# Kernel tuning notes

Hardware: AMD Instinct MI355X
Metric: run time of the kernel (lower is better)

Reference implementation:

```python
import jax, jax.numpy as jnp
import numpy as np

N, E = 50000, 640000
FEAT, EMB, HID, B = 128, 128, 512, 32


def setup_inputs() -> dict:
    key = jax.random.key(0)
    ks = jax.random.split(key, 12)
    def w(k, shape, fan_in):
        return jax.random.normal(k, shape, dtype=jnp.float32) / np.sqrt(fan_in)
    return {
        "x": jax.random.normal(ks[0], (N, FEAT), dtype=jnp.float32),
        "edge_index": jax.random.randint(ks[1], (2, E), 0, N, dtype=jnp.int64),
        "last_hidden": jax.random.normal(ks[2], (1, B, HID), dtype=jnp.float32),
        "W1_rel": w(ks[3], (FEAT, EMB), FEAT),
        "W1_root": w(ks[4], (FEAT, EMB), FEAT),
        "b1": jnp.zeros((EMB,), dtype=jnp.float32),
        "W2_rel": w(ks[5], (EMB, EMB), EMB),
        "W2_root": w(ks[6], (EMB, EMB), EMB),
        "b2": jnp.zeros((EMB,), dtype=jnp.float32),
        "Wp": w(ks[7], (HID, EMB), HID),
        "bp": jnp.zeros((EMB,), dtype=jnp.float32),
    }


def _rgcn(h, src, dst, W_rel, W_root, b):
    # transform-then-gather (N < E so cheaper): messages along edges src->dst
    msg = (h @ W_rel)[src]                                   # [E, emb]
    agg = jax.ops.segment_sum(msg, dst, num_segments=N)      # [N, emb]
    deg = jax.ops.segment_sum(jnp.ones((E,), h.dtype), dst, num_segments=N)
    agg = agg / jnp.maximum(deg, 1.0)[:, None]               # mean aggregation (PyG RGCNConv default)
    return agg + h @ W_root + b


def reference(x, edge_index, last_hidden, W1_rel, W1_root, b1, W2_rel, W2_root, b2, Wp, bp):
    src, dst = edge_index[0], edge_index[1]
    h = jax.nn.relu(_rgcn(x, src, dst, W1_rel, W1_root, b1))   # [N, emb]
    h = jax.nn.relu(_rgcn(h, src, dst, W2_rel, W2_root, b2))   # [N, emb]
    message_embed = (last_hidden @ Wp + bp)[0]                 # squeeze(0) -> [B, emb]
    scores = h @ message_embed.T                               # [N, B]
    return jax.nn.log_softmax(scores, axis=0)
```

## Files before the change

### kernel.cpp

```cpp
#include <hip/hip_runtime.h>
#include <hip/hip_bf16.h>

#define N_NODES 50000
#define N_EDGES 640000
#define DUMMY   N_NODES
#define PAD_SSRC 990000

typedef __attribute__((ext_vector_type(8))) short short8;
typedef __attribute__((ext_vector_type(4))) float floatx4;

__device__ __forceinline__ float bf2f(unsigned short u) {
    return __uint_as_float(((unsigned int)u) << 16);
}
__device__ __forceinline__ unsigned short f2bf(float x) {
    unsigned int u = __float_as_uint(x);
    u = (u + 0x7fffu + ((u >> 16) & 1u)) >> 16;
    return (unsigned short)u;
}
__device__ __forceinline__ unsigned char f2f8(float x) {
    int pk = __builtin_amdgcn_cvt_pk_fp8_f32(x, x, 0, false);
    return (unsigned char)(pk & 0xff);
}

__global__ void __launch_bounds__(256) prep_k(const float* __restrict__ W0,
                                              const float* __restrict__ W1,
                                              const float* __restrict__ W2,
                                              const float* __restrict__ W3,
                                              unsigned short* __restrict__ T0,
                                              unsigned short* __restrict__ T1,
                                              unsigned short* __restrict__ T2,
                                              unsigned short* __restrict__ T3,
                                              int* __restrict__ cnt,
                                              const float* __restrict__ lh,
                                              const float* __restrict__ Wp,
                                              const float* __restrict__ bp,
                                              unsigned short* __restrict__ meb,
                                              unsigned short* __restrict__ ssrc,
                                              unsigned char* __restrict__ tbf,
                                              int* __restrict__ total,
                                              const int* __restrict__ dst,
                                              int* __restrict__ rank) {
    int b = blockIdx.x, tid = threadIdx.x;
    bool is_hist;
    int idx;
    if (b < 4414) { is_hist = ((b & 1) == 0); idx = b >> 1; }
    else          { is_hist = true;            idx = 2207 + (b - 4414); }
    if (is_hist) {
        int e = idx * 256 + tid;
        int d = dst[e];
        int r = atomicAdd(&cnt[d], 1);
        rank[e] = (r << 16) | d;
        return;
    }
    int s = idx;
    if (s < 256) {
        int i2 = s * 256 + tid;
        int w = i2 >> 14;
        int r = i2 & 16383;
        int n = r >> 7, k = r & 127;
        const float* W = (w == 0) ? W0 : (w == 1) ? W1 : (w == 2) ? W2 : W3;
        unsigned short* T = (w == 0) ? T0 : (w == 1) ? T1 : (w == 2) ? T2 : T3;
        T[r] = f2bf(W[k * 128 + n]);
    } else if (s < 272) {
        int o = (s - 256) * 256 + tid;
        int i = o >> 7, c = o & 127;
        float acc = bp[c];
        const float4* lr = (const float4*)(lh + i * 512);
        #pragma unroll 4
        for (int k4 = 0; k4 < 128; k4++) {
            float4 v = lr[k4];
            acc += v.x * Wp[(4 * k4 + 0) * 128 + c] + v.y * Wp[(4 * k4 + 1) * 128 + c]
                 + v.z * Wp[(4 * k4 + 2) * 128 + c] + v.w * Wp[(4 * k4 + 3) * 128 + c];
        }
        meb[o] = f2bf(acc);
    } else if (s < 2206) {
        int i = (s - 272) * 256 + tid;
        if (i < PAD_SSRC / 2) ((unsigned int*)ssrc)[i] = 0xC350C350u;
    } else {
        if (tid < 32) ((unsigned int*)(tbf + (size_t)DUMMY * 128))[tid] = 0;
        else if (tid == 32) *total = 0;
    }
}

template <bool AF32>
__device__ __forceinline__ void gemm_dual_body(int bid, int tid,
                                               const void* __restrict__ Ain,
                                               const unsigned short* __restrict__ BtRel,
                                               const unsigned short* __restrict__ BtRoot,
                                               unsigned char* __restrict__ Trel,
                                               unsigned short* __restrict__ Rootb, int M) {
    int wid = tid >> 6, lane = tid & 63;
    int r0 = bid * 64 + wid * 16;
    int m = lane & 15, g = lane >> 4;
    int row = r0 + m;
    int rowc = (row < M) ? row : (M - 1);
    short8 a[4];
    if constexpr (AF32) {
        const float* A = (const float*)Ain;
        #pragma unroll
        for (int kt = 0; kt < 4; kt++) {
            const float* p = A + (size_t)rowc * 128 + kt * 32 + g * 8;
            float4 v0 = *(const float4*)p;
            float4 v1 = *(const float4*)(p + 4);
            short8 t;
            t[0] = (short)f2bf(v0.x); t[1] = (short)f2bf(v0.y);
            t[2] = (short)f2bf(v0.z); t[3] = (short)f2bf(v0.w);
            t[4] = (short)f2bf(v1.x); t[5] = (short)f2bf(v1.y);
            t[6] = (short)f2bf(v1.z); t[7] = (short)f2bf(v1.w);
            a[kt] = t;
        }
    } else {
        const unsigned short* A = (const unsigned short*)Ain;
        #pragma unroll
        for (int kt = 0; kt < 4; kt++)
            a[kt] = *(const short8*)(A + (size_t)rowc * 128 + kt * 32 + g * 8);
    }
    floatx4 accR[8], accO[8];
    #pragma unroll
    for (int ct = 0; ct < 8; ct++) {
        accR[ct] = (floatx4)(0.f);
        accO[ct] = (floatx4)(0.f);
    }
    #pragma unroll
    for (int ct = 0; ct < 8; ct++) {
        const unsigned short* br = BtRel  + (size_t)(ct * 16 + m) * 128 + g * 8;
        const unsigned short* bo = BtRoot + (size_t)(ct * 16 + m) * 128 + g * 8;
        #pragma unroll
        for (int kt = 0; kt < 4; kt++) {
            short8 bR = *(const short8*)(br + kt * 32);
            accR[ct] = __builtin_amdgcn_mfma_f32_16x16x32_bf16(a[kt], bR, accR[ct], 0, 0, 0);
            short8 bO = *(const short8*)(bo + kt * 32);
            accO[ct] = __builtin_amdgcn_mfma_f32_16x16x32_bf16(a[kt], bO, accO[ct], 0, 0, 0);
        }
    }
    #pragma unroll
    for (int ct = 0; ct < 8; ct++) {
        #pragma unroll
        for (int rg = 0; rg < 4; rg++) {
            int ro = r0 + g * 4 + rg;
            if (ro < M) {
                int co = ct * 16 + m;
                Trel[(size_t)ro * 128 + co]  = f2f8(accR[ct][rg]);
                Rootb[(size_t)ro * 128 + co] = f2bf(accO[ct][rg]);
            }
        }
    }
}

__global__ void __launch_bounds__(256) allocgemm_k(const int* __restrict__ cnt,
                                                   int* __restrict__ prow,
                                                   int* __restrict__ total,
                                                   const float* __restrict__ A,
                                                   const unsigned short* __restrict__ BtRel,
                                                   const unsigned short* __restrict__ BtRoot,
                                                   unsigned char* __restrict__ Trel,
                                                   unsigned short* __restrict__ Rootb) {
    if (blockIdx.x < 196) {
        __shared__ int sm[256];
        __shared__ int base_s;
        int t = threadIdx.x;
        int i = blockIdx.x * 256 + t;
        int pc = (i < N_NODES) ? ((cnt[i] + 7) & ~7) : 0;
        sm[t] = pc;
        __syncthreads();
        for (int off = 1; off < 256; off <<= 1) {
            int v = (t >= off) ? sm[t - off] : 0;
            __syncthreads();
            sm[t] += v;
            __syncthreads();
        }
        if (t == 255) base_s = atomicAdd(total, sm[255]);
        __syncthreads();
        if (i < N_NODES) prow[i] = base_s + sm[t] - pc;
    } else {
        gemm_dual_body<true>(blockIdx.x - 196, threadIdx.x, A, BtRel, BtRoot, Trel, Rootb, N_NODES);
    }
}

__global__ void __launch_bounds__(256) place_k(const int* __restrict__ src,
                                               const int* __restrict__ prow,
                                               const int* __restrict__ rank,
                                               unsigned short* __restrict__ ssrc) {
    int e = blockIdx.x * 256 + threadIdx.x;
    if (e < N_EDGES) {
        int pk = rank[e];
        int d = pk & 0xffff;
        int r = pk >> 16;
        ssrc[prow[d] + r] = (unsigned short)src[e];
    }
}

__global__ void __launch_bounds__(256) gemm_dual_k(const unsigned short* __restrict__ A,
                                                   const unsigned short* __restrict__ BtRel,
                                                   const unsigned short* __restrict__ BtRoot,
                                                   unsigned char* __restrict__ Trel,
                                                   unsigned short* __restrict__ Rootb, int M) {
    gemm_dual_body<false>(blockIdx.x, threadIdx.x, A, BtRel, BtRoot, Trel, Rootb, M);
}

__global__ void __launch_bounds__(256) agg_k(const int* __restrict__ prow,
                                             const int* __restrict__ cnt,
                                             const unsigned short* __restrict__ ssrc,
                                             const unsigned char* __restrict__ t,
                                             const unsigned short* __restrict__ rootb,
                                             const float* __restrict__ bias,
                                             unsigned short* __restrict__ hout) {
    int node = blockIdx.x * 4 + (threadIdx.x >> 6);
    if (node >= N_NODES) return;
    int lane = threadIdx.x & 63;
    int fl = lane & 31;
    int sh = (lane & 32) >> 1;
    int beg = prow[node];
    int deg = cnt[node];
    int endp = beg + ((deg + 7) & ~7);
    const unsigned char* tf = t + fl * 4;
    float a0=0.f,a1=0.f,a2=0.f,a3=0.f;
    float b0=0.f,b1=0.f,b2=0.f,b3=0.f;
    for (int e = beg; e < endp; e += 16) {
        uint4 w0 = *(const uint4*)(ssrc + e);
        uint4 w1 = (e + 8 < endp) ? *(const uint4*)(ssrc + e + 8)
                                  : make_uint4(0xC350C350u, 0xC350C350u, 0xC350C350u, 0xC350C350u);
        int i0 = (int)((w0.x >> sh) & 0xffffu);
        int i1 = (int)((w0.y >> sh) & 0xffffu);
        int i2 = (int)((w0.z >> sh) & 0xffffu);
        int i3 = (int)((w0.w >> sh) & 0xffffu);
        int i4 = (int)((w1.x >> sh) & 0xffffu);
        int i5 = (int)((w1.y >> sh) & 0xffffu);
        int i6 = (int)((w1.z >> sh) & 0xffffu);
        int i7 = (int)((w1.w >> sh) & 0xffffu);
        unsigned int u0 = *(const unsigned int*)(tf + (size_t)i0 * 128);
        unsigned int u1 = *(const unsigned int*)(tf + (size_t)i1 * 128);
        unsigned int u2 = *(const unsigned int*)(tf + (size_t)i2 * 128);
        unsigned int u3 = *(const unsigned int*)(tf + (size_t)i3 * 128);
        unsigned int u4 = *(const unsigned int*)(tf + (size_t)i4 * 128);
        unsigned int u5 = *(const unsigned int*)(tf + (size_t)i5 * 128);
        unsigned int u6 = *(const unsigned int*)(tf + (size_t)i6 * 128);
        unsigned int u7 = *(const unsigned int*)(tf + (size_t)i7 * 128);
        a0 += __builtin_amdgcn_cvt_f32_fp8(u0, 0) + __builtin_amdgcn_cvt_f32_fp8(u1, 0);
        a1 += __builtin_amdgcn_cvt_f32_fp8(u0, 1) + __builtin_amdgcn_cvt_f32_fp8(u1, 1);
        a2 += __builtin_amdgcn_cvt_f32_fp8(u0, 2) + __builtin_amdgcn_cvt_f32_fp8(u1, 2);
        a3 += __builtin_amdgcn_cvt_f32_fp8(u0, 3) + __builtin_amdgcn_cvt_f32_fp8(u1, 3);
        b0 += __builtin_amdgcn_cvt_f32_fp8(u2, 0) + __builtin_amdgcn_cvt_f32_fp8(u3, 0);
        b1 += __builtin_amdgcn_cvt_f32_fp8(u2, 1) + __builtin_amdgcn_cvt_f32_fp8(u3, 1);
        b2 += __builtin_amdgcn_cvt_f32_fp8(u2, 2) + __builtin_amdgcn_cvt_f32_fp8(u3, 2);
        b3 += __builtin_amdgcn_cvt_f32_fp8(u2, 3) + __builtin_amdgcn_cvt_f32_fp8(u3, 3);
        a0 += __builtin_amdgcn_cvt_f32_fp8(u4, 0) + __builtin_amdgcn_cvt_f32_fp8(u5, 0);
        a1 += __builtin_amdgcn_cvt_f32_fp8(u4, 1) + __builtin_amdgcn_cvt_f32_fp8(u5, 1);
        a2 += __builtin_amdgcn_cvt_f32_fp8(u4, 2) + __builtin_amdgcn_cvt_f32_fp8(u5, 2);
        a3 += __builtin_amdgcn_cvt_f32_fp8(u4, 3) + __builtin_amdgcn_cvt_f32_fp8(u5, 3);
        b0 += __builtin_amdgcn_cvt_f32_fp8(u6, 0) + __builtin_amdgcn_cvt_f32_fp8(u7, 0);
        b1 += __builtin_amdgcn_cvt_f32_fp8(u6, 1) + __builtin_amdgcn_cvt_f32_fp8(u7, 1);
        b2 += __builtin_amdgcn_cvt_f32_fp8(u6, 2) + __builtin_amdgcn_cvt_f32_fp8(u7, 2);
        b3 += __builtin_amdgcn_cvt_f32_fp8(u6, 3) + __builtin_amdgcn_cvt_f32_fp8(u7, 3);
    }
    a0 += b0; a1 += b1; a2 += b2; a3 += b3;
    a0 += __shfl_xor(a0, 32);
    a1 += __shfl_xor(a1, 32);
    a2 += __shfl_xor(a2, 32);
    a3 += __shfl_xor(a3, 32);
    if ((lane & 32) == 0) {
        float inv = 1.f / fmaxf((float)deg, 1.f);
        int f = fl * 4;
        ushort4 r = *(const ushort4*)(rootb + (size_t)node * 128 + f);
        float4 bb = *(const float4*)(bias + f);
        ushort4 o;
        o.x = f2bf(fmaxf(a0 * inv + bf2f(r.x) + bb.x, 0.f));
        o.y = f2bf(fmaxf(a1 * inv + bf2f(r.y) + bb.y, 0.f));
        o.z = f2bf(fmaxf(a2 * inv + bf2f(r.z) + bb.z, 0.f));
        o.w = f2bf(fmaxf(a3 * inv + bf2f(r.w) + bb.w, 0.f));
        *(ushort4*)(hout + (size_t)node * 128 + f) = o;
    }
}

__global__ void __launch_bounds__(256) scores_cs_k(const unsigned short* __restrict__ A,
                                                   const unsigned short* __restrict__ Bt,
                                                   float* __restrict__ S,
                                                   float* __restrict__ pm,
                                                   float* __restrict__ ps) {
    __shared__ float Sl[64][33];
    __shared__ float sm[256], ss[256];
    int tid = threadIdx.x;
    int wid = tid >> 6, lane = tid & 63;
    int r0 = blockIdx.x * 64 + wid * 16;
    int m = lane & 15, g = lane >> 4;
    int row = r0 + m;
    int rowc = (row < N_NODES) ? row : (N_NODES - 1);
    short8 a[4];
    #pragma unroll
    for (int kt = 0; kt < 4; kt++)
        a[kt] = *(const short8*)(A + (size_t)rowc * 128 + kt * 32 + g * 8);
    floatx4 acc[2];
    acc[0] = (floatx4)(0.f);
    acc[1] = (floatx4)(0.f);
    #pragma unroll
    for (int ct = 0; ct < 2; ct++) {
        const unsigned short* b = Bt + (size_t)(ct * 16 + m) * 128 + g * 8;
        #pragma unroll
        for (int kt = 0; kt < 4; kt++) {
            short8 bv = *(const short8*)(b + kt * 32);
            acc[ct] = __builtin_amdgcn_mfma_f32_16x16x32_bf16(a[kt], bv, acc[ct], 0, 0, 0);
        }
    }
    #pragma unroll
    for (int ct = 0; ct < 2; ct++) {
        #pragma unroll
        for (int rg = 0; rg < 4; rg++) {
            int lr = wid * 16 + g * 4 + rg;
            int ro = r0 + g * 4 + rg;
            Sl[lr][ct * 16 + m] = acc[ct][rg];
            if (ro < N_NODES) S[(size_t)ro * 32 + ct * 16 + m] = acc[ct][rg];
        }
    }
    __syncthreads();
    int col = tid & 31, sub = tid >> 5;
    int blkbase = blockIdx.x * 64;
    float mm = -3.4e38f, s = 0.f;
    for (int r = sub; r < 64; r += 8) {
        if (blkbase + r < N_NODES) {
            float v = Sl[r][col];
            if (v > mm) { s = s * __expf(mm - v) + 1.f; mm = v; }
            else        { s += __expf(v - mm); }
        }
    }
    sm[tid] = mm; ss[tid] = s;
    __syncthreads();
    for (int off = 128; off >= 32; off >>= 1) {
        if (tid < off) {
            float m2 = sm[tid + off], s2 = ss[tid + off];
            float M = fmaxf(sm[tid], m2);
            ss[tid] = ss[tid] * __expf(sm[tid] - M) + s2 * __expf(m2 - M);
            sm[tid] = M;
        }
        __syncthreads();
    }
    if (tid < 32) { pm[tid * 782 + blockIdx.x] = sm[tid]; ps[tid * 782 + blockIdx.x] = ss[tid]; }
}

__global__ void __launch_bounds__(256) merge_k(const float* __restrict__ pm,
                                               const float* __restrict__ ps,
                                               float* __restrict__ cmg,
                                               float* __restrict__ clg) {
    __shared__ float sm[256], ss[256];
    int col = blockIdx.x;
    int t = threadIdx.x;
    float m = -3.4e38f, s = 0.f;
    for (int c = t; c < 782; c += 256) {
        float m2 = pm[col * 782 + c], s2 = ps[col * 782 + c];
        float M = fmaxf(m, m2);
        s = s * __expf(m - M) + s2 * __expf(m2 - M);
        m = M;
    }
    sm[t] = m; ss[t] = s;
    __syncthreads();
    for (int off = 128; off > 0; off >>= 1) {
        if (t < off) {
            float m2 = sm[t + off], s2 = ss[t + off];
            float M = fmaxf(sm[t], m2);
            ss[t] = ss[t] * __expf(sm[t] - M) + s2 * __expf(m2 - M);
            sm[t] = M;
        }
        __syncthreads();
    }
    if (t == 0) { cmg[col] = sm[0]; clg[col] = logf(ss[0]); }
}

__global__ void __launch_bounds__(256) final_k(const float* __restrict__ S,
                                               const float* __restrict__ cmg,
                                               const float* __restrict__ clg,
                                               float* __restrict__ out) {
    __shared__ float cc[32];
    int t = threadIdx.x;
    if (t < 32) cc[t] = cmg[t] + clg[t];
    __syncthreads();
    int idx = blockIdx.x * 256 + t;
    if (idx < N_NODES * 32) {
        int b = idx & 31;
        out[idx] = S[idx] - cc[b];
    }
}

extern "C" void kernel_launch(void* const* d_in, const int* in_sizes, int n_in,
                              void* d_out, int out_size, void* d_ws, size_t ws_size,
                              hipStream_t stream) {
    const float* x       = (const float*)d_in[0];
    const int*   ei      = (const int*)d_in[1];
    const float* lh      = (const float*)d_in[2];
    const float* W1_rel  = (const float*)d_in[3];
    const float* W1_root = (const float*)d_in[4];
    const float* b1      = (const float*)d_in[5];
    const float* W2_rel  = (const float*)d_in[6];
    const float* W2_root = (const float*)d_in[7];
    const float* b2      = (const float*)d_in[8];
    const float* Wp      = (const float*)d_in[9];
    const float* bp      = (const float*)d_in[10];
    float* out = (float*)d_out;
    float* ws  = (float*)d_ws;

    unsigned char*  tbf   = (unsigned char*)(ws + 3200000);
    unsigned short* rootb = (unsigned short*)(ws + 4800032);
    unsigned short* hb    = (unsigned short*)(ws + 8000032);
    unsigned short* Wt1r  = (unsigned short*)(ws + 11200032);
    unsigned short* Wt1o  = (unsigned short*)(ws + 11208224);
    unsigned short* Wt2r  = (unsigned short*)(ws + 11216416);
    unsigned short* Wt2o  = (unsigned short*)(ws + 11224608);
    unsigned short* MEb   = (unsigned short*)(ws + 11232800);
    float* pm   = ws + 11234848;
    float* ps   = ws + 11259872;
    float* cmg  = ws + 11284896;
    float* clg  = ws + 11284928;
    int*   cnt  = (int*)(ws + 11284960);
    int*   prow = (int*)(ws + 11334960);
    int*   total= (int*)(ws + 11384961);
    int*   rank = (int*)(ws + 11384964);
    unsigned short* ssrc = (unsigned short*)(ws + 12024964);
    float* S    = ws + 12519964;

    const int* srcp = ei;
    const int* dstp = ei + N_EDGES;

    const int e_grid   = (N_EDGES + 255) / 256;
    const int ew_grid  = (N_NODES * 32 + 255) / 256;
    const int agg_grid = (N_NODES + 3) / 4;
    const int mm_grid  = (N_NODES + 63) / 64;

    hipMemsetAsync(cnt, 0, N_NODES * sizeof(int), stream);

    prep_k<<<4707, 256, 0, stream>>>(W1_rel, W1_root, W2_rel, W2_root,
                                     Wt1r, Wt1o, Wt2r, Wt2o,
                                     cnt, lh, Wp, bp, MEb, ssrc, tbf, total,
                                     dstp, rank);

    allocgemm_k<<<196 + mm_grid, 256, 0, stream>>>(cnt, prow, total,
                                                   x, Wt1r, Wt1o, tbf, rootb);

    place_k<<<e_grid, 256, 0, stream>>>(srcp, prow, rank, ssrc);

    agg_k<<<agg_grid, 256, 0, stream>>>(prow, cnt, ssrc, tbf, rootb, b1, hb);

    gemm_dual_k<<<mm_grid, 256, 0, stream>>>(hb, Wt2r, Wt2o, tbf, rootb, N_NODES);

    agg_k<<<agg_grid, 256, 0, stream>>>(prow, cnt, ssrc, tbf, rootb, b2, hb);

    scores_cs_k<<<mm_grid, 256, 0, stream>>>(hb, MEb, S, pm, ps);

    merge_k<<<32, 256, 0, stream>>>(pm, ps, cmg, clg);

    final_k<<<ew_grid, 256, 0, stream>>>(S, cmg, clg, out);
}
```

Baseline: 263.6 us.

## Reschedule prep kernels: fold memset, overlap histogram with layer-1 GEMM, LDS-staged layer-2 GEMM

The cnt memset moves into a new prep0 kernel alongside weight transposes. The edge histogram is now interleaved with the layer-1 dual GEMM in one kernel, and the prefix-sum allocation becomes its own small kernel. The layer-2 GEMM stages the transposed weights through swizzled LDS, running rel and root in two phases with one accumulator set. This changes launch count and overlap patterns and may alter register pressure, but adds an extra launch for alloc.

```diff
diff --git a/kernel.cpp b/kernel.cpp
--- a/kernel.cpp
+++ b/kernel.cpp
@@ -22,47 +22,36 @@
     return (unsigned char)(pk & 0xff);
 }
 
-__global__ void __launch_bounds__(256) prep_k(const float* __restrict__ W0,
-                                              const float* __restrict__ W1,
-                                              const float* __restrict__ W2,
-                                              const float* __restrict__ W3,
-                                              unsigned short* __restrict__ T0,
-                                              unsigned short* __restrict__ T1,
-                                              unsigned short* __restrict__ T2,
-                                              unsigned short* __restrict__ T3,
-                                              int* __restrict__ cnt,
-                                              const float* __restrict__ lh,
-                                              const float* __restrict__ Wp,
-                                              const float* __restrict__ bp,
-                                              unsigned short* __restrict__ meb,
-                                              unsigned short* __restrict__ ssrc,
-                                              unsigned char* __restrict__ tbf,
-                                              int* __restrict__ total,
-                                              const int* __restrict__ dst,
-                                              int* __restrict__ rank) {
+__global__ void __launch_bounds__(256) prep0_k(const float* __restrict__ W0,
+                                               const float* __restrict__ W1,
+                                               const float* __restrict__ W2,
+                                               const float* __restrict__ W3,
+                                               unsigned short* __restrict__ T0,
+                                               unsigned short* __restrict__ T1,
+                                               unsigned short* __restrict__ T2,
+                                               unsigned short* __restrict__ T3,
+                                               int* __restrict__ cnt,
+                                               const float* __restrict__ lh,
+                                               const float* __restrict__ Wp,
+                                               const float* __restrict__ bp,
+                                               unsigned short* __restrict__ meb,
+                                               unsigned short* __restrict__ ssrc,
+                                               unsigned char* __restrict__ tbf,
+                                               int* __restrict__ total) {
     int b = blockIdx.x, tid = threadIdx.x;
-    bool is_hist;
-    int idx;
-    if (b < 4414) { is_hist = ((b & 1) == 0); idx = b >> 1; }
-    else          { is_hist = true;            idx = 2207 + (b - 4414); }
-    if (is_hist) {
-        int e = idx * 256 + tid;
-        int d = dst[e];
-        int r = atomicAdd(&cnt[d], 1);
-        rank[e] = (r << 16) | d;
-        return;
-    }
-    int s = idx;
-    if (s < 256) {
-        int i2 = s * 256 + tid;
+    if (b < 196) {
+        int i = b * 256 + tid;
+        if (i < N_NODES) cnt[i] = 0;
+    } else if (b < 452) {
+        int i2 = (b - 196) * 256 + tid;
         int w = i2 >> 14;
         int r = i2 & 16383;
         int n = r >> 7, k = r & 127;
         const float* W = (w == 0) ? W0 : (w == 1) ? W1 : (w == 2) ? W2 : W3;
         unsigned short* T = (w == 0) ? T0 : (w == 1) ? T1 : (w == 2) ? T2 : T3;
         T[r] = f2bf(W[k * 128 + n]);
-    } else if (s < 272) {
-        int o = (s - 256) * 256 + tid;
+    } else if (b < 468) {
+        int o = (b - 452) * 256 + tid;
         int i = o >> 7, c = o & 127;
         float acc = bp[c];
         const float4* lr = (const float4*)(lh + i * 512);
@@ -73,8 +62,8 @@
                  + v.z * Wp[(4 * k4 + 2) * 128 + c] + v.w * Wp[(4 * k4 + 3) * 128 + c];
         }
         meb[o] = f2bf(acc);
-    } else if (s < 2206) {
-        int i = (s - 272) * 256 + tid;
+    } else if (b < 2402) {
+        int i = (b - 468) * 256 + tid;
         if (i < PAD_SSRC / 2) ((unsigned int*)ssrc)[i] = 0xC350C350u;
     } else {
         if (tid < 32) ((unsigned int*)(tbf + (size_t)DUMMY * 128))[tid] = 0;
@@ -147,34 +136,52 @@
     }
 }
 
-__global__ void __launch_bounds__(256) allocgemm_k(const int* __restrict__ cnt,
-                                                   int* __restrict__ prow,
-                                                   int* __restrict__ total,
-                                                   const float* __restrict__ A,
-                                                   const unsigned short* __restrict__ BtRel,
-                                                   const unsigned short* __restrict__ BtRoot,
-                                                   unsigned char* __restrict__ Trel,
-                                                   unsigned short* __restrict__ Rootb) {
-    if (blockIdx.x < 196) {
-        __shared__ int sm[256];
-        __shared__ int base_s;
-        int t = threadIdx.x;
-        int i = blockIdx.x * 256 + t;
-        int pc = (i < N_NODES) ? ((cnt[i] + 7) & ~7) : 0;
-        sm[t] = pc;
+__global__ void __launch_bounds__(256) prep1_k(int* __restrict__ cnt,
+                                               const int* __restrict__ dst,
+                                               int* __restrict__ rank,
+                                               const float* __restrict__ A,
+                                               const unsigned short* __restrict__ BtRel,
+                                               const unsigned short* __restrict__ BtRoot,
+                                               unsigned char* __restrict__ Trel,
+                                               unsigned short* __restrict__ Rootb) {
+    int b = blockIdx.x, tid = threadIdx.x;
+    bool is_gemm = false;
+    int idx;
+    if (b < 3128) {
+        if ((b & 3) == 3) { is_gemm = true;  idx = b >> 2; }
+        else              {                  idx = (b >> 2) * 3 + (b & 3); }
+    } else {
+        idx = 2346 + (b - 3128);
+    }
+    if (is_gemm) {
+        gemm_dual_body<true>(idx, tid, A, BtRel, BtRoot, Trel, Rootb, N_NODES);
+    } else {
+        int e = idx * 256 + tid;
+        int d = dst[e];
+        int r = atomicAdd(&cnt[d], 1);
+        rank[e] = (r << 16) | d;
+    }
+}
+
+__global__ void __launch_bounds__(256) alloc_k(const int* __restrict__ cnt,
+                                               int* __restrict__ prow,
+                                               int* __restrict__ total) {
+    __shared__ int sm[256];
+    __shared__ int base_s;
+    int t = threadIdx.x;
+    int i = blockIdx.x * 256 + t;
+    int pc = (i < N_NODES) ? ((cnt[i] + 7) & ~7) : 0;
+    sm[t] = pc;
+    __syncthreads();
+    for (int off = 1; off < 256; off <<= 1) {
+        int v = (t >= off) ? sm[t - off] : 0;
         __syncthreads();
-        for (int off = 1; off < 256; off <<= 1) {
-            int v = (t >= off) ? sm[t - off] : 0;
-            __syncthreads();
-            sm[t] += v;
-            __syncthreads();
-        }
-        if (t == 255) base_s = atomicAdd(total, sm[255]);
+        sm[t] += v;
         __syncthreads();
-        if (i < N_NODES) prow[i] = base_s + sm[t] - pc;
-    } else {
-        gemm_dual_body<true>(blockIdx.x - 196, threadIdx.x, A, BtRel, BtRoot, Trel, Rootb, N_NODES);
-    }
+    }
+    if (t == 255) base_s = atomicAdd(total, sm[255]);
+    __syncthreads();
+    if (i < N_NODES) prow[i] = base_s + sm[t] - pc;
 }
 
 __global__ void __launch_bounds__(256) place_k(const int* __restrict__ src,
@@ -190,12 +197,63 @@
     }
 }
 
-__global__ void __launch_bounds__(256) gemm_dual_k(const unsigned short* __restrict__ A,
-                                                   const unsigned short* __restrict__ BtRel,
-                                                   const unsigned short* __restrict__ BtRoot,
-                                                   unsigned char* __restrict__ Trel,
-                                                   unsigned short* __restrict__ Rootb, int M) {
-    gemm_dual_body<false>(blockIdx.x, threadIdx.x, A, BtRel, BtRoot, Trel, Rootb, M);
+__global__ void __launch_bounds__(256) gemm_dual_lds_k(const unsigned short* __restrict__ A,
+                                                       const unsigned short* __restrict__ BtRel,
+                                                       const unsigned short* __restrict__ BtRoot,
+                                                       unsigned char* __restrict__ Trel,
+                                                       unsigned short* __restrict__ Rootb, int M) {
+    __shared__ __align__(16) unsigned short Bl[16384];
+    int tid = threadIdx.x;
+    int wid = tid >> 6, lane = tid & 63;
+    int r0 = blockIdx.x * 64 + wid * 16;
+    int m = lane & 15, g = lane >> 4;
+    int row = r0 + m;
+    int rowc = (row < M) ? row : (M - 1);
+    short8 a[4];
+    #pragma unroll
+    for (int kt = 0; kt < 4; kt++)
+        a[kt] = *(const short8*)(A + (size_t)rowc * 128 + kt * 32 + g * 8);
+
+    #pragma unroll
+    for (int ph = 0; ph < 2; ph++) {
+        const unsigned short* Bt = ph ? BtRoot : BtRel;
+        if (ph) __syncthreads();
+        #pragma unroll
+        for (int j = 0; j < 8; j++) {
+            int eo = j * 2048 + tid * 8;
+            short8 v = *(const short8*)(Bt + eo);
+            int swz = (eo * 2) ^ (((eo >> 7) & 7) << 4);
+            *(short8*)((char*)Bl + swz) = v;
+        }
+        __syncthreads();
+        floatx4 acc[8];
+        #pragma unroll
+        for (int ct = 0; ct < 8; ct++) acc[ct] = (floatx4)(0.f);
+        #pragma unroll
+        for (int ct = 0; ct < 8; ct++) {
+            int br = ct * 16 + m;
+            int base = br * 256;
+            int sw = (br & 7) << 4;
+            #pragma unroll
+            for (int kt = 0; kt < 4; kt++) {
+                int byte = (base + kt * 64 + g * 16) ^ sw;
+                short8 bv = *(const short8*)((const char*)Bl + byte);
+                acc[ct] = __builtin_amdgcn_mfma_f32_16x16x32_bf16(a[kt], bv, acc[ct], 0, 0, 0);
+            }
+        }
+        #pragma unroll
+        for (int ct = 0; ct < 8; ct++) {
+            #pragma unroll
+            for (int rg = 0; rg < 4; rg++) {
+                int ro = r0 + g * 4 + rg;
+                if (ro < M) {
+                    int co = ct * 16 + m;
+                    if (ph == 0) Trel[(size_t)ro * 128 + co]  = f2f8(acc[ct][rg]);
+                    else         Rootb[(size_t)ro * 128 + co] = f2bf(acc[ct][rg]);
+                }
+            }
+        }
+    }
 }
 
 __global__ void __launch_bounds__(256) agg_k(const int* __restrict__ prow,
@@ -423,21 +481,20 @@
     const int agg_grid = (N_NODES + 3) / 4;
     const int mm_grid  = (N_NODES + 63) / 64;
 
-    hipMemsetAsync(cnt, 0, N_NODES * sizeof(int), stream);
-
-    prep_k<<<4707, 256, 0, stream>>>(W1_rel, W1_root, W2_rel, W2_root,
-                                     Wt1r, Wt1o, Wt2r, Wt2o,
-                                     cnt, lh, Wp, bp, MEb, ssrc, tbf, total,
-                                     dstp, rank);
-
-    allocgemm_k<<<196 + mm_grid, 256, 0, stream>>>(cnt, prow, total,
-                                                   x, Wt1r, Wt1o, tbf, rootb);
+    prep0_k<<<2403, 256, 0, stream>>>(W1_rel, W1_root, W2_rel, W2_root,
+                                      Wt1r, Wt1o, Wt2r, Wt2o,
+                                      cnt, lh, Wp, bp, MEb, ssrc, tbf, total);
+
+    prep1_k<<<3128 + 154, 256, 0, stream>>>(cnt, dstp, rank,
+                                            x, Wt1r, Wt1o, tbf, rootb);
+
+    alloc_k<<<196, 256, 0, stream>>>(cnt, prow, total);
 
     place_k<<<e_grid, 256, 0, stream>>>(srcp, prow, rank, ssrc);
 
     agg_k<<<agg_grid, 256, 0, stream>>>(prow, cnt, ssrc, tbf, rootb, b1, hb);
 
-    gemm_dual_k<<<mm_grid, 256, 0, stream>>>(hb, Wt2r, Wt2o, tbf, rootb, N_NODES);
+    gemm_dual_lds_k<<<mm_grid, 256, 0, stream>>>(hb, Wt2r, Wt2o, tbf, rootb, N_NODES);
 
     agg_k<<<agg_grid, 256, 0, stream>>>(prow, cnt, ssrc, tbf, rootb, b2, hb);
 
```

Result: slower. 313.3 us (+18.9%).
